# Kernel tuning notes

Measured on AMD Instinct MI355X. Metric: run time of the kernel, lower is better.

Reference implementation:

```python
import jax, jax.numpy as jnp
import numpy as np

N_NODES = 50000
N_EDGES = 800000
IN_CH = 128
HID = 64
N_LAYERS = 14
EPS_MSG = 1e-7
EPS_SM = 1e-16
LN_EPS = 1e-5


def setup_inputs() -> dict:
    key = jax.random.key(0)
    ks = jax.random.split(key, 8)
    x = jax.random.normal(ks[0], (N_NODES, IN_CH), dtype=jnp.float32)
    edge_index = jax.random.randint(ks[1], (2, N_EDGES), 0, N_NODES, dtype=jnp.int64)
    enc_W = jax.random.normal(ks[2], (IN_CH, HID), dtype=jnp.float32) / np.sqrt(IN_CH)
    enc_b = jnp.zeros((HID,), dtype=jnp.float32)
    mlp_W = jax.random.normal(ks[3], (N_LAYERS, HID, HID), dtype=jnp.float32) / np.sqrt(HID)
    mlp_b = jnp.zeros((N_LAYERS, HID), dtype=jnp.float32)
    t = jnp.ones((N_LAYERS,), dtype=jnp.float32)  # learn_t, init t=1.0
    return {"x": x, "edge_index": edge_index, "enc_W": enc_W, "enc_b": enc_b,
            "mlp_W": mlp_W, "mlp_b": mlp_b, "t": t}


def _layernorm(h):
    # LayerNorm(elementwise_affine=False) over last dim
    mu = jnp.mean(h, axis=-1, keepdims=True)
    var = jnp.mean((h - mu) ** 2, axis=-1, keepdims=True)
    return (h - mu) * jax.lax.rsqrt(var + LN_EPS)


def _segment_softmax(scores, seg, num_segments):
    # per-target-node, per-channel softmax over incoming edges
    m = jax.ops.segment_max(scores, seg, num_segments=num_segments)
    e = jnp.exp(scores - m[seg])
    s = jax.ops.segment_sum(e, seg, num_segments=num_segments)
    return e / (s[seg] + EPS_SM)


def _genconv(h, src, dst, W, b, t):
    # GENConv: msg = relu(x_j) + eps; softmax_sg aggregation (weights detached);
    # out = MLP(aggr + x) where MLP is a single Linear
    msg = jax.nn.relu(h[src]) + EPS_MSG                       # [E, H]
    alpha = _segment_softmax(t * msg, dst, N_NODES)           # [E, H]
    alpha = jax.lax.stop_gradient(alpha)                      # 'softmax_sg'
    aggr = jax.ops.segment_sum(msg * alpha, dst, num_segments=N_NODES)
    return (aggr + h) @ W + b


def reference(x, edge_index, enc_W, enc_b, mlp_W, mlp_b, t):
    src, dst = edge_index[0], edge_index[1]
    h = x @ enc_W + enc_b                                     # node encoder
    h = _genconv(h, src, dst, mlp_W[0], mlp_b[0], t[0])       # layers[0].conv

    def body(carry, params):
        W, b, tt = params
        y = jax.nn.relu(_layernorm(carry))                    # res+ pre-norm/act
        y = _genconv(y, src, dst, W, b, tt)                   # dropout inactive (eval)
        return carry + y, None

    h, _ = jax.lax.scan(body, h, (mlp_W[1:], mlp_b[1:], t[1:]))
    h = jax.nn.relu(_layernorm(h))                            # final norm + act
    return jax.nn.log_softmax(h, axis=-1)
```

## Files before the change

### kernel.cpp

```cpp
#include <hip/hip_runtime.h>

#define NN 50000
#define NE 800000
#define INC 128
#define HIDC 64
#define NL 14
#define EPS_MSG 1e-7f
#define EPS_SM 1e-16f
#define LN_EPS 1e-5f

#define SCAN_B 256
#define NB_SCAN ((NN + SCAN_B - 1) / SCAN_B)

__device__ __forceinline__ float wave_sum(float v) {
    #pragma unroll
    for (int o = 32; o > 0; o >>= 1) v += __shfl_xor(v, o, 64);
    return v;
}
__device__ __forceinline__ float wave_max(float v) {
    #pragma unroll
    for (int o = 32; o > 0; o >>= 1) v = fmaxf(v, __shfl_xor(v, o, 64));
    return v;
}
__device__ __forceinline__ unsigned pack_bf2(float lo, float hi) {
    unsigned ul = __float_as_uint(lo); ul += 0x7fffu + ((ul >> 16) & 1u);
    unsigned uh = __float_as_uint(hi); uh += 0x7fffu + ((uh >> 16) & 1u);
    return (ul >> 16) | (uh & 0xffff0000u);
}

__global__ void k_hist(const int* __restrict__ dst, int* __restrict__ deg) {
    int i = blockIdx.x * blockDim.x + threadIdx.x;
    if (i < NE) atomicAdd(&deg[dst[i]], 1);
}

__global__ void k_part(const int* __restrict__ deg, int* __restrict__ part) {
    __shared__ int sm[SCAN_B];
    int b = blockIdx.x;
    int i = b * SCAN_B + threadIdx.x;
    sm[threadIdx.x] = (i < NN) ? deg[i] : 0;
    __syncthreads();
    for (int s = SCAN_B / 2; s > 0; s >>= 1) {
        if (threadIdx.x < s) sm[threadIdx.x] += sm[threadIdx.x + s];
        __syncthreads();
    }
    if (threadIdx.x == 0) part[b] = sm[0];
}

__global__ void k_scanpart(const int* __restrict__ part, int* __restrict__ partOfs) {
    __shared__ int sm[SCAN_B];
    int t = threadIdx.x;
    int own = (t < NB_SCAN) ? part[t] : 0;
    sm[t] = own;
    __syncthreads();
    for (int o = 1; o < SCAN_B; o <<= 1) {
        int v = (t >= o) ? sm[t - o] : 0;
        __syncthreads();
        sm[t] += v;
        __syncthreads();
    }
    if (t < NB_SCAN) partOfs[t] = sm[t] - own;
}

__global__ void k_scanfinal(const int* __restrict__ deg, const int* __restrict__ partOfs,
                            int* __restrict__ rowOfs) {
    __shared__ int sm[SCAN_B];
    int b = blockIdx.x, t = threadIdx.x;
    int i = b * SCAN_B + t;
    int d = (i < NN) ? deg[i] : 0;
    sm[t] = d;
    __syncthreads();
    for (int o = 1; o < SCAN_B; o <<= 1) {
        int v = (t >= o) ? sm[t - o] : 0;
        __syncthreads();
        sm[t] += v;
        __syncthreads();
    }
    if (i < NN) rowOfs[i] = partOfs[b] + sm[t] - d;
    if (i == 0) rowOfs[NN] = NE;
}

__global__ void k_scatter(const int* __restrict__ src, const int* __restrict__ dst,
                          const int* __restrict__ rowOfs, int* __restrict__ cur,
                          int* __restrict__ csr) {
    int i = blockIdx.x * blockDim.x + threadIdx.x;
    if (i < NE) {
        int d = dst[i];
        int p = rowOfs[d] + atomicAdd(&cur[d], 1);
        csr[p] = src[i];
    }
}

__global__ __launch_bounds__(256) void k_enc(const float* __restrict__ x,
                                             const float* __restrict__ W,
                                             const float* __restrict__ bias,
                                             float* __restrict__ h,
                                             unsigned* __restrict__ B0) {
    __shared__ float XL[32 * INC];
    __shared__ float WL[INC * HIDC];
    int tid = threadIdx.x;
    for (int i = tid; i < (INC * HIDC) / 4; i += 256)
        ((float4*)WL)[i] = ((const float4*)W)[i];
    int r0 = blockIdx.x * 32;
    for (int i = tid; i < (32 * INC) / 4; i += 256) {
        int row = i >> 5;
        float4 val = make_float4(0.f, 0.f, 0.f, 0.f);
        if (r0 + row < NN) val = ((const float4*)x)[(size_t)(r0 + row) * 32 + (i & 31)];
        ((float4*)XL)[i] = val;
    }
    __syncthreads();
    int lane = tid & 63, w = tid >> 6;
    float bv = bias[lane];
    #pragma unroll
    for (int i = 0; i < 4; i++) {
        int ra = w * 8 + i * 2, rb = ra + 1;
        float a0 = 0.f, a1 = 0.f, a2 = 0.f, a3 = 0.f;
        float c0 = 0.f, c1 = 0.f, c2 = 0.f, c3 = 0.f;
        #pragma unroll
        for (int k = 0; k < INC; k += 4) {
            float4 xa = *(const float4*)&XL[ra * INC + k];
            float4 xb = *(const float4*)&XL[rb * INC + k];
            float w0 = WL[(k + 0) * HIDC + lane];
            float w1 = WL[(k + 1) * HIDC + lane];
            float w2 = WL[(k + 2) * HIDC + lane];
            float w3 = WL[(k + 3) * HIDC + lane];
            a0 = fmaf(xa.x, w0, a0); a1 = fmaf(xa.y, w1, a1);
            a2 = fmaf(xa.z, w2, a2); a3 = fmaf(xa.w, w3, a3);
            c0 = fmaf(xb.x, w0, c0); c1 = fmaf(xb.y, w1, c1);
            c2 = fmaf(xb.z, w2, c2); c3 = fmaf(xb.w, w3, c3);
        }
        int ga = r0 + ra, gb = r0 + rb;
        float va = bv + ((a0 + a1) + (a2 + a3));
        float vb = bv + ((c0 + c1) + (c2 + c3));
        float pa = __shfl_xor(va, 1, 64);
        float pb = __shfl_xor(vb, 1, 64);
        if (ga < NN) {
            h[(size_t)ga * HIDC + lane] = va;
            if (!(lane & 1)) B0[(size_t)ga * 32 + (lane >> 1)] = pack_bf2(va, pa);
        }
        if (gb < NN) {
            h[(size_t)gb * HIDC + lane] = vb;
            if (!(lane & 1)) B0[(size_t)gb * 32 + (lane >> 1)] = pack_bf2(vb, pb);
        }
    }
}

template<bool FIRST, bool FINAL>
__global__ __launch_bounds__(256) void k_layer(const float* __restrict__ henc,
                                               float* __restrict__ h,
                                               const unsigned* __restrict__ Bin,
                                               unsigned* __restrict__ Bout,
                                               const int* __restrict__ rowOfs,
                                               const int* __restrict__ csr,
                                               const float* __restrict__ W,
                                               const float* __restrict__ b,
                                               const float* __restrict__ tptr) {
    __shared__ float WL[HIDC * HIDC];
    for (int i = threadIdx.x; i < (HIDC * HIDC) / 4; i += 256)
        ((float4*)WL)[i] = ((const float4*)W)[i];
    __syncthreads();

    int lane = threadIdx.x & 63;
    int v = (blockIdx.x * 256 + threadIdx.x) >> 6;
    int g = lane >> 4;
    int c = lane & 15;
    float t = *tptr;
    float tl = t * 1.44269504088896f;

    int e0 = rowOfs[v], e1 = rowOfs[v + 1];
    float se0 = 0.f, se1 = 0.f, se2 = 0.f, se3 = 0.f;
    float sw0 = 0.f, sw1 = 0.f, sw2 = 0.f, sw3 = 0.f;
    for (int e = e0; e < e1; e += 16) {
        #pragma unroll
        for (int j = 0; j < 4; j++) {
            int ee = e + 4 * j + g;
            bool valid = ee < e1;
            int s = csr[valid ? ee : e0];
            uint2 q = ((const uint2*)Bin)[(size_t)s * 16 + c];
            float g0 = __uint_as_float(q.x << 16);
            float g1 = __uint_as_float(q.x & 0xffff0000u);
            float g2 = __uint_as_float(q.y << 16);
            float g3 = __uint_as_float(q.y & 0xffff0000u);
            g0 = fmaxf(g0, 0.f) + EPS_MSG;
            g1 = fmaxf(g1, 0.f) + EPS_MSG;
            g2 = fmaxf(g2, 0.f) + EPS_MSG;
            g3 = fmaxf(g3, 0.f) + EPS_MSG;
            float w0 = valid ? exp2f(tl * g0) : 0.f;
            float w1 = valid ? exp2f(tl * g1) : 0.f;
            float w2 = valid ? exp2f(tl * g2) : 0.f;
            float w3 = valid ? exp2f(tl * g3) : 0.f;
            se0 += w0; sw0 = fmaf(g0, w0, sw0);
            se1 += w1; sw1 = fmaf(g1, w1, sw1);
            se2 += w2; sw2 = fmaf(g2, w2, sw2);
            se3 += w3; sw3 = fmaf(g3, w3, sw3);
        }
    }
    #pragma unroll
    for (int m = 16; m <= 32; m <<= 1) {
        se0 += __shfl_xor(se0, m, 64); sw0 += __shfl_xor(sw0, m, 64);
        se1 += __shfl_xor(se1, m, 64); sw1 += __shfl_xor(sw1, m, 64);
        se2 += __shfl_xor(se2, m, 64); sw2 += __shfl_xor(sw2, m, 64);
        se3 += __shfl_xor(se3, m, 64); sw3 += __shfl_xor(sw3, m, 64);
    }
    float ax = sw0 / (se0 + EPS_SM);
    float ay = sw1 / (se1 + EPS_SM);
    float az = sw2 / (se2 + EPS_SM);
    float aw = sw3 / (se3 + EPS_SM);

    float base = b[lane];
    if (FIRST) {
        float4 s4 = ((const float4*)henc)[(size_t)v * 16 + c];
        ax += s4.x; ay += s4.y; az += s4.z; aw += s4.w;
    } else {
        float4 hv4 = ((const float4*)h)[(size_t)v * 16 + c];
        float ls = (hv4.x + hv4.y) + (hv4.z + hv4.w);
        #pragma unroll
        for (int m = 1; m <= 8; m <<= 1) ls += __shfl_xor(ls, m, 64);
        float mu = ls * (1.f / 64.f);
        float dx = hv4.x - mu, dy = hv4.y - mu, dz = hv4.z - mu, dw = hv4.w - mu;
        float vs = (dx * dx + dy * dy) + (dz * dz + dw * dw);
        #pragma unroll
        for (int m = 1; m <= 8; m <<= 1) vs += __shfl_xor(vs, m, 64);
        float rs = rsqrtf(vs * (1.f / 64.f) + LN_EPS);
        ax += fmaxf(dx * rs, 0.f); ay += fmaxf(dy * rs, 0.f);
        az += fmaxf(dz * rs, 0.f); aw += fmaxf(dw * rs, 0.f);
        base += h[(size_t)v * HIDC + lane];
    }

    float a0 = 0.f, a1 = 0.f, a2 = 0.f, a3 = 0.f;
    #pragma unroll
    for (int k = 0; k < 64; k += 4) {
        float b0 = __shfl(ax, k >> 2, 64);
        float b1 = __shfl(ay, k >> 2, 64);
        float b2 = __shfl(az, k >> 2, 64);
        float b3 = __shfl(aw, k >> 2, 64);
        a0 = fmaf(b0, WL[(k + 0) * HIDC + lane], a0);
        a1 = fmaf(b1, WL[(k + 1) * HIDC + lane], a1);
        a2 = fmaf(b2, WL[(k + 2) * HIDC + lane], a2);
        a3 = fmaf(b3, WL[(k + 3) * HIDC + lane], a3);
    }
    float acc = base + ((a0 + a1) + (a2 + a3));

    if (FINAL) {
        float mu = wave_sum(acc) * (1.f / 64.f);
        float d = acc - mu;
        float var = wave_sum(d * d) * (1.f / 64.f);
        float z = fmaxf(d * rsqrtf(var + LN_EPS), 0.f);
        float m = wave_max(z);
        float s2 = wave_sum(exp2f((z - m) * 1.44269504088896f));
        h[(size_t)v * HIDC + lane] = z - (m + __logf(s2));
    } else {
        h[(size_t)v * HIDC + lane] = acc;
        float mu = wave_sum(acc) * (1.f / 64.f);
        float d = acc - mu;
        float var = wave_sum(d * d) * (1.f / 64.f);
        float y = fmaxf(d * rsqrtf(var + LN_EPS), 0.f);
        float yp = __shfl_xor(y, 1, 64);
        if (!(lane & 1)) Bout[(size_t)v * 32 + (lane >> 1)] = pack_bf2(y, yp);
    }
}

extern "C" void kernel_launch(void* const* d_in, const int* in_sizes, int n_in,
                              void* d_out, int out_size, void* d_ws, size_t ws_size,
                              hipStream_t stream) {
    const float* x    = (const float*)d_in[0];
    const int*   ei   = (const int*)d_in[1];
    const float* encW = (const float*)d_in[2];
    const float* encb = (const float*)d_in[3];
    const float* mlpW = (const float*)d_in[4];
    const float* mlpb = (const float*)d_in[5];
    const float* t    = (const float*)d_in[6];

    float* h = (float*)d_out;

    char* ws = (char*)d_ws;
    size_t off = 0;
    auto alloc = [&](size_t bytes) -> void* {
        void* p = ws + off;
        off += (bytes + 255) / 256 * 256;
        return p;
    };
    float*    henc   = (float*)alloc((size_t)NN * HIDC * 4);
    unsigned* B0     = (unsigned*)alloc((size_t)NN * 32 * 4);
    unsigned* B1     = (unsigned*)alloc((size_t)NN * 32 * 4);
    int*      deg    = (int*)alloc((size_t)NN * 4);
    int*      cur    = (int*)alloc((size_t)NN * 4);
    int*      rowOfs = (int*)alloc((size_t)(NN + 1) * 4);
    int*      part   = (int*)alloc((size_t)NB_SCAN * 4);
    int*      partOf = (int*)alloc((size_t)NB_SCAN * 4);
    int*      csr    = (int*)alloc((size_t)NE * 4);

    const int* src = ei;
    const int* dst = ei + NE;

    hipMemsetAsync(deg, 0, (size_t)NN * 4, stream);
    hipMemsetAsync(cur, 0, (size_t)NN * 4, stream);

    k_hist<<<(NE + 255) / 256, 256, 0, stream>>>(dst, deg);
    k_part<<<NB_SCAN, SCAN_B, 0, stream>>>(deg, part);
    k_scanpart<<<1, SCAN_B, 0, stream>>>(part, partOf);
    k_scanfinal<<<NB_SCAN, SCAN_B, 0, stream>>>(deg, partOf, rowOfs);
    k_scatter<<<(NE + 255) / 256, 256, 0, stream>>>(src, dst, rowOfs, cur, csr);

    k_enc<<<(NN + 31) / 32, 256, 0, stream>>>(x, encW, encb, henc, B0);

    k_layer<true, false><<<12500, 256, 0, stream>>>(henc, h, B0, B1, rowOfs, csr,
                                                    mlpW, mlpb, t);
    for (int l = 1; l < NL - 1; l++) {
        const float* W  = mlpW + (size_t)l * HIDC * HIDC;
        const float* bb = mlpb + (size_t)l * HIDC;
        unsigned* Bi = (l & 1) ? B1 : B0;
        unsigned* Bo = (l & 1) ? B0 : B1;
        k_layer<false, false><<<12500, 256, 0, stream>>>(nullptr, h, Bi, Bo, rowOfs, csr,
                                                         W, bb, t + l);
    }
    k_layer<false, true><<<12500, 256, 0, stream>>>(nullptr, h, B1, nullptr, rowOfs, csr,
                                                    mlpW + (size_t)(NL - 1) * HIDC * HIDC,
                                                    mlpb + (size_t)(NL - 1) * HIDC,
                                                    t + (NL - 1));
}
```

Measured before the change: 1.237 ms.

## Split fused layer kernel into edge-aggregation and persistent node-MLP kernels

Each fused per-layer kernel becomes two: a gather/softmax aggregation kernel that writes the aggregate to a float buffer, and a grid-strided MLP kernel that loads the weight matrix into shared memory once per block and applies residual LayerNorm, the matvec (with readlane broadcasts) and the output norm. The goal is to stop every 4-wave block from reloading the 16KB weight matrix and to let the aggregation kernel run without shared memory, raising its occupancy. In exchange it adds an extra float round trip of the aggregate through global memory and twice as many launches per layer.

New measurement: 1.089 ms. 11.9% less time.

```diff
diff --git a/kernel.cpp b/kernel.cpp
--- a/kernel.cpp
+++ b/kernel.cpp
@@ -21,6 +21,9 @@
     #pragma unroll
     for (int o = 32; o > 0; o >>= 1) v = fmaxf(v, __shfl_xor(v, o, 64));
     return v;
+}
+__device__ __forceinline__ float bcast(float x, int l) {
+    return __int_as_float(__builtin_amdgcn_readlane(__float_as_int(x), l));
 }
 __device__ __forceinline__ unsigned pack_bf2(float lo, float hi) {
     unsigned ul = __float_as_uint(lo); ul += 0x7fffu + ((ul >> 16) & 1u);
@@ -144,27 +147,18 @@
     }
 }
 
-template<bool FIRST, bool FINAL>
-__global__ __launch_bounds__(256) void k_layer(const float* __restrict__ henc,
-                                               float* __restrict__ h,
-                                               const unsigned* __restrict__ Bin,
-                                               unsigned* __restrict__ Bout,
-                                               const int* __restrict__ rowOfs,
-                                               const int* __restrict__ csr,
-                                               const float* __restrict__ W,
-                                               const float* __restrict__ b,
-                                               const float* __restrict__ tptr) {
-    __shared__ float WL[HIDC * HIDC];
-    for (int i = threadIdx.x; i < (HIDC * HIDC) / 4; i += 256)
-        ((float4*)WL)[i] = ((const float4*)W)[i];
-    __syncthreads();
-
+template<bool FIRST>
+__global__ __launch_bounds__(256) void k_aggr(const float* __restrict__ henc,
+                                              const unsigned* __restrict__ Bin,
+                                              const int* __restrict__ rowOfs,
+                                              const int* __restrict__ csr,
+                                              const float* __restrict__ tptr,
+                                              float* __restrict__ A) {
     int lane = threadIdx.x & 63;
     int v = (blockIdx.x * 256 + threadIdx.x) >> 6;
     int g = lane >> 4;
     int c = lane & 15;
-    float t = *tptr;
-    float tl = t * 1.44269504088896f;
+    float tl = (*tptr) * 1.44269504088896f;
 
     int e0 = rowOfs[v], e1 = rowOfs[v + 1];
     float se0 = 0.f, se1 = 0.f, se2 = 0.f, se3 = 0.f;
@@ -201,61 +195,74 @@
         se2 += __shfl_xor(se2, m, 64); sw2 += __shfl_xor(sw2, m, 64);
         se3 += __shfl_xor(se3, m, 64); sw3 += __shfl_xor(sw3, m, 64);
     }
-    float ax = sw0 / (se0 + EPS_SM);
-    float ay = sw1 / (se1 + EPS_SM);
-    float az = sw2 / (se2 + EPS_SM);
-    float aw = sw3 / (se3 + EPS_SM);
-
-    float base = b[lane];
-    if (FIRST) {
-        float4 s4 = ((const float4*)henc)[(size_t)v * 16 + c];
-        ax += s4.x; ay += s4.y; az += s4.z; aw += s4.w;
-    } else {
-        float4 hv4 = ((const float4*)h)[(size_t)v * 16 + c];
-        float ls = (hv4.x + hv4.y) + (hv4.z + hv4.w);
+    if (g == 0) {
+        float4 r;
+        r.x = sw0 / (se0 + EPS_SM);
+        r.y = sw1 / (se1 + EPS_SM);
+        r.z = sw2 / (se2 + EPS_SM);
+        r.w = sw3 / (se3 + EPS_SM);
+        if (FIRST) {
+            float4 s4 = ((const float4*)henc)[(size_t)v * 16 + c];
+            r.x += s4.x; r.y += s4.y; r.z += s4.z; r.w += s4.w;
+        }
+        ((float4*)A)[(size_t)v * 16 + c] = r;
+    }
+}
+
+template<bool LNRES, int MODE>
+__global__ __launch_bounds__(256) void k_mlp(const float* __restrict__ A,
+                                             float* __restrict__ h,
+                                             unsigned* __restrict__ Bout,
+                                             const float* __restrict__ W,
+                                             const float* __restrict__ b) {
+    __shared__ float WL[HIDC * HIDC];
+    for (int i = threadIdx.x; i < (HIDC * HIDC) / 4; i += 256)
+        ((float4*)WL)[i] = ((const float4*)W)[i];
+    __syncthreads();
+
+    int lane = threadIdx.x & 63;
+    int wid = (blockIdx.x * 256 + threadIdx.x) >> 6;
+    int nw = (gridDim.x * 256) >> 6;
+    float bv = b[lane];
+
+    for (int v = wid; v < NN; v += nw) {
+        float a = A[(size_t)v * HIDC + lane];
+        float base = bv;
+        if (LNRES) {
+            float hv = h[(size_t)v * HIDC + lane];
+            float mu = wave_sum(hv) * (1.f / 64.f);
+            float d = hv - mu;
+            float var = wave_sum(d * d) * (1.f / 64.f);
+            a += fmaxf(d * rsqrtf(var + LN_EPS), 0.f);
+            base += hv;
+        }
+        float a0 = 0.f, a1 = 0.f, a2 = 0.f, a3 = 0.f;
         #pragma unroll
-        for (int m = 1; m <= 8; m <<= 1) ls += __shfl_xor(ls, m, 64);
-        float mu = ls * (1.f / 64.f);
-        float dx = hv4.x - mu, dy = hv4.y - mu, dz = hv4.z - mu, dw = hv4.w - mu;
-        float vs = (dx * dx + dy * dy) + (dz * dz + dw * dw);
-        #pragma unroll
-        for (int m = 1; m <= 8; m <<= 1) vs += __shfl_xor(vs, m, 64);
-        float rs = rsqrtf(vs * (1.f / 64.f) + LN_EPS);
-        ax += fmaxf(dx * rs, 0.f); ay += fmaxf(dy * rs, 0.f);
-        az += fmaxf(dz * rs, 0.f); aw += fmaxf(dw * rs, 0.f);
-        base += h[(size_t)v * HIDC + lane];
-    }
-
-    float a0 = 0.f, a1 = 0.f, a2 = 0.f, a3 = 0.f;
-    #pragma unroll
-    for (int k = 0; k < 64; k += 4) {
-        float b0 = __shfl(ax, k >> 2, 64);
-        float b1 = __shfl(ay, k >> 2, 64);
-        float b2 = __shfl(az, k >> 2, 64);
-        float b3 = __shfl(aw, k >> 2, 64);
-        a0 = fmaf(b0, WL[(k + 0) * HIDC + lane], a0);
-        a1 = fmaf(b1, WL[(k + 1) * HIDC + lane], a1);
-        a2 = fmaf(b2, WL[(k + 2) * HIDC + lane], a2);
-        a3 = fmaf(b3, WL[(k + 3) * HIDC + lane], a3);
-    }
-    float acc = base + ((a0 + a1) + (a2 + a3));
-
-    if (FINAL) {
-        float mu = wave_sum(acc) * (1.f / 64.f);
-        float d = acc - mu;
-        float var = wave_sum(d * d) * (1.f / 64.f);
-        float z = fmaxf(d * rsqrtf(var + LN_EPS), 0.f);
-        float m = wave_max(z);
-        float s2 = wave_sum(exp2f((z - m) * 1.44269504088896f));
-        h[(size_t)v * HIDC + lane] = z - (m + __logf(s2));
-    } else {
-        h[(size_t)v * HIDC + lane] = acc;
-        float mu = wave_sum(acc) * (1.f / 64.f);
-        float d = acc - mu;
-        float var = wave_sum(d * d) * (1.f / 64.f);
-        float y = fmaxf(d * rsqrtf(var + LN_EPS), 0.f);
-        float yp = __shfl_xor(y, 1, 64);
-        if (!(lane & 1)) Bout[(size_t)v * 32 + (lane >> 1)] = pack_bf2(y, yp);
+        for (int k = 0; k < 64; k += 4) {
+            a0 = fmaf(bcast(a, k + 0), WL[(k + 0) * HIDC + lane], a0);
+            a1 = fmaf(bcast(a, k + 1), WL[(k + 1) * HIDC + lane], a1);
+            a2 = fmaf(bcast(a, k + 2), WL[(k + 2) * HIDC + lane], a2);
+            a3 = fmaf(bcast(a, k + 3), WL[(k + 3) * HIDC + lane], a3);
+        }
+        float acc = base + ((a0 + a1) + (a2 + a3));
+
+        if (MODE == 1) {
+            float mu = wave_sum(acc) * (1.f / 64.f);
+            float d = acc - mu;
+            float var = wave_sum(d * d) * (1.f / 64.f);
+            float z = fmaxf(d * rsqrtf(var + LN_EPS), 0.f);
+            float m = wave_max(z);
+            float s2 = wave_sum(exp2f((z - m) * 1.44269504088896f));
+            h[(size_t)v * HIDC + lane] = z - (m + __logf(s2));
+        } else {
+            h[(size_t)v * HIDC + lane] = acc;
+            float mu = wave_sum(acc) * (1.f / 64.f);
+            float d = acc - mu;
+            float var = wave_sum(d * d) * (1.f / 64.f);
+            float y = fmaxf(d * rsqrtf(var + LN_EPS), 0.f);
+            float yp = __shfl_xor(y, 1, 64);
+            if (!(lane & 1)) Bout[(size_t)v * 32 + (lane >> 1)] = pack_bf2(y, yp);
+        }
     }
 }
 
@@ -280,6 +287,7 @@
         return p;
     };
     float*    henc   = (float*)alloc((size_t)NN * HIDC * 4);
+    float*    A      = (float*)alloc((size_t)NN * HIDC * 4);
     unsigned* B0     = (unsigned*)alloc((size_t)NN * 32 * 4);
     unsigned* B1     = (unsigned*)alloc((size_t)NN * 32 * 4);
     int*      deg    = (int*)alloc((size_t)NN * 4);
@@ -303,18 +311,19 @@
 
     k_enc<<<(NN + 31) / 32, 256, 0, stream>>>(x, encW, encb, henc, B0);
 
-    k_layer<true, false><<<12500, 256, 0, stream>>>(henc, h, B0, B1, rowOfs, csr,
-                                                    mlpW, mlpb, t);
+    k_aggr<true><<<12500, 256, 0, stream>>>(henc, B0, rowOfs, csr, t, A);
+    k_mlp<false, 0><<<2048, 256, 0, stream>>>(A, h, B1, mlpW, mlpb);
+
     for (int l = 1; l < NL - 1; l++) {
-        const float* W  = mlpW + (size_t)l * HIDC * HIDC;
-        const float* bb = mlpb + (size_t)l * HIDC;
         unsigned* Bi = (l & 1) ? B1 : B0;
         unsigned* Bo = (l & 1) ? B0 : B1;
-        k_layer<false, false><<<12500, 256, 0, stream>>>(nullptr, h, Bi, Bo, rowOfs, csr,
-                                                         W, bb, t + l);
-    }
-    k_layer<false, true><<<12500, 256, 0, stream>>>(nullptr, h, B1, nullptr, rowOfs, csr,
-                                                    mlpW + (size_t)(NL - 1) * HIDC * HIDC,
-                                                    mlpb + (size_t)(NL - 1) * HIDC,
-                                                    t + (NL - 1));
-}
+        k_aggr<false><<<12500, 256, 0, stream>>>(nullptr, Bi, rowOfs, csr, t + l, A);
+        k_mlp<true, 0><<<2048, 256, 0, stream>>>(A, h, Bo,
+                                                 mlpW + (size_t)l * HIDC * HIDC,
+                                                 mlpb + (size_t)l * HIDC);
+    }
+    k_aggr<false><<<12500, 256, 0, stream>>>(nullptr, B1, rowOfs, csr, t + (NL - 1), A);
+    k_mlp<true, 1><<<2048, 256, 0, stream>>>(A, h, nullptr,
+                                             mlpW + (size_t)(NL - 1) * HIDC * HIDC,
+                                             mlpb + (size_t)(NL - 1) * HIDC);
+}
```
